# Kernel tuning notes

Measured on AMD Instinct MI355X. Metric: run time of the kernel, lower is better.

The kernel has to match this reference:

```python
import jax, jax.numpy as jnp
import numpy as np

B, C_IN, H, W = 4, 256, 48, 48
HEADS, HD = 8, 64
N = H * W
SCALE = 1.0 / (HD ** 0.5)


def setup_inputs() -> dict:
    key = jax.random.key(0)
    ks = jax.random.split(key, 5)
    x = jax.random.normal(ks[0], (B, C_IN, H, W), dtype=jnp.float32)
    # 1x1 conv weights, squeezed: [heads, head_channels, in_channels]
    Wq = jax.random.normal(ks[1], (HEADS, HD, C_IN), dtype=jnp.float32) * (C_IN ** -0.5)
    Wk = jax.random.normal(ks[2], (HEADS, HD, C_IN), dtype=jnp.float32) * (C_IN ** -0.5)
    Wv = jax.random.normal(ks[3], (HEADS, HD, C_IN), dtype=jnp.float32) * (C_IN ** -0.5)
    # output 1x1 conv: [in_channels, heads*head_channels]
    Wo = jax.random.normal(ks[4], (C_IN, HEADS * HD), dtype=jnp.float32) * ((HEADS * HD) ** -0.5)
    return {"x": x, "Wq": Wq, "Wk": Wk, "Wv": Wv, "Wo": Wo}


def reference(x, Wq, Wk, Wv, Wo):
    b, c, h, w = x.shape
    n = h * w
    xf = x.reshape(b, c, n)  # [B, C, N]
    # per-head 1x1 convs == batched projections -> [heads, B, N, HD]
    q = jnp.einsum('hdc,bcn->hbnd', Wq, xf)
    k = jnp.einsum('hdc,bcn->hbnd', Wk, xf)
    v = jnp.einsum('hdc,bcn->hbnd', Wv, xf)
    scores = jnp.einsum('hbnd,hbmd->hbnm', q, k) * SCALE  # [heads, B, N, N]
    probs = jax.nn.softmax(scores, axis=-1)
    ws = jnp.einsum('hbnm,hbmd->hbnd', probs, v)  # [heads, B, N, HD]
    # faithful replication of torch: transpose(1,2) then reshape(B, heads*HD, H, W)
    ws = jnp.transpose(ws, (0, 2, 1, 3))  # [heads, N, B, HD]
    ws = ws.reshape(b, HEADS * HD, h, w)
    out = jnp.einsum('oc,bchw->bohw', Wo, ws)  # output 1x1 conv
    return out
```

## Files before the change

kernel.cpp:

```cpp
#include <hip/hip_runtime.h>

#define B_     4
#define CIN    256
#define NTOK   2304
#define HEADS  8
#define HD     64
#define SCALE  0.125f
#define LOG2E  1.44269504088896f
#define QSCALE (SCALE * LOG2E)
#define PBIAS  4.0f
#define QKV_ELEMS (HEADS * B_ * NTOK * HD)
#define HBSTRIDE 147456
#define WSZ    131072

typedef _Float16 f16;
typedef _Float16 __attribute__((ext_vector_type(8))) h8v;
typedef _Float16 __attribute__((ext_vector_type(4))) h4v;
typedef ushort   __attribute__((ext_vector_type(8))) us8;
typedef float    __attribute__((ext_vector_type(16))) f16v;

__device__ inline uint pk2(float a, float b) {
    auto v = __builtin_amdgcn_cvt_pkrtz(a, b);
    return __builtin_bit_cast(uint, v);
}
#define EXP2(x) __builtin_amdgcn_exp2f(x)

#define GLOAD_LDS(g, l) __builtin_amdgcn_global_load_lds( \
    (const __attribute__((address_space(1))) unsigned int*)(g), \
    (__attribute__((address_space(3))) unsigned int*)(l), 16, 0, 0)

__global__ __launch_bounds__(256) void castw(
    const float* __restrict__ Wq, const float* __restrict__ Wk,
    const float* __restrict__ Wv, const float* __restrict__ Wo,
    f16* __restrict__ wc, f16* __restrict__ woc)
{
    int e4 = (blockIdx.x * 256 + threadIdx.x) * 4;
    const float* src; f16* dst; float mult = 1.0f; int off;
    if (e4 < WSZ)          { src = Wq; off = e4;           dst = wc;           mult = QSCALE; }
    else if (e4 < 2 * WSZ) { src = Wk; off = e4 - WSZ;     dst = wc + WSZ; }
    else if (e4 < 3 * WSZ) { src = Wv; off = e4 - 2 * WSZ; dst = wc + 2 * WSZ; }
    else                   { src = Wo; off = e4 - 3 * WSZ; dst = woc; }
    float4 r = *(const float4*)(src + off);
    h4v hv;
    hv.x = (f16)(r.x * mult); hv.y = (f16)(r.y * mult);
    hv.z = (f16)(r.z * mult); hv.w = (f16)(r.w * mult);
    *(h4v*)(dst + off) = hv;
}

__global__ __launch_bounds__(256) void tcastf(
    const float* __restrict__ src, f16* __restrict__ dst, int C)
{
    const int n0 = blockIdx.x * 64;
    const int c0 = blockIdx.y * 64;
    const int b  = blockIdx.z;
    __shared__ float T[64][65];
    const int tid = threadIdx.x;
    const float* sb = src + ((size_t)b * C + c0) * NTOK;
    #pragma unroll
    for (int i = 0; i < 16; ++i) {
        int idx = tid + 256 * i;
        int rr = idx >> 6, ll = idx & 63;
        T[ll][rr] = sb[(size_t)rr * NTOK + n0 + ll];
    }
    __syncthreads();
    const size_t ob = ((size_t)b * NTOK + n0) * C + c0;
    #pragma unroll
    for (int i = 0; i < 4; ++i) {
        int idx = tid + 256 * i;
        int row = idx >> 4, c4 = (idx & 15) * 4;
        h4v v;
        v.x = (f16)T[row][c4 + 0]; v.y = (f16)T[row][c4 + 1];
        v.z = (f16)T[row][c4 + 2]; v.w = (f16)T[row][c4 + 3];
        *(h4v*)(dst + ob + (size_t)row * C + c4) = v;
    }
}

__global__ __launch_bounds__(128) void proj_mfma(
    const f16* __restrict__ wc, const f16* __restrict__ xt,
    f16* __restrict__ qh, f16* __restrict__ kh, f16* __restrict__ vth)
{
    const int ntile = blockIdx.x;
    const int hp    = blockIdx.y;
    const int b     = blockIdx.z;
    const int p     = hp >> 3, h = hp & 7;
    const int hb    = h * 4 + b;
    const f16* Wp = wc + ((size_t)p * 8 + h) * (HD * CIN);

    __shared__ __align__(16) f16 Ws[2][64][64], Xs[2][64][64];

    const int tid = threadIdx.x;
    const int w = tid >> 6, lane = tid & 63;
    const int lm = lane & 31, lh = lane >> 5;
    const int n_loc  = w * 32 + lm;
    const int n_glob = ntile * 64 + n_loc;

    const f16* xb = xt + ((size_t)b * NTOK + ntile * 64) * CIN;

    auto stage = [&](int buf, int c0) {
        const f16* src = (w == 0) ? Wp : xb;
        f16* dst = (w == 0) ? &Ws[buf][0][0] : &Xs[buf][0][0];
        #pragma unroll
        for (int i = 0; i < 8; ++i) {
            int g = i * 64 + lane; int row = g >> 3; int c = (g & 7) ^ (row & 7);
            GLOAD_LDS(src + (size_t)row * CIN + c0 + c * 8, dst + i * 512);
        }
    };

    f16v o0, o1;
    #pragma unroll
    for (int i = 0; i < 16; ++i) { o0[i] = 0.f; o1[i] = 0.f; }

    stage(0, 0);
    for (int c0 = 0; c0 < CIN; c0 += 64) {
        const int cur = (c0 >> 6) & 1;
        __syncthreads();
        if (c0 + 64 < CIN) stage(cur ^ 1, c0 + 64);
        #pragma unroll
        for (int s = 0; s < 4; ++s) {
            const int pp = ((2 * s + lh) ^ (lm & 7)) * 8;
            h8v a0 = *(const h8v*)&Ws[cur][lm][pp];
            h8v a1 = *(const h8v*)&Ws[cur][lm + 32][pp];
            h8v bh = *(const h8v*)&Xs[cur][n_loc][pp];
            o0 = __builtin_amdgcn_mfma_f32_32x32x16_f16(a0, bh, o0, 0, 0, 0);
            o1 = __builtin_amdgcn_mfma_f32_32x32x16_f16(a1, bh, o1, 0, 0, 0);
        }
    }

    const size_t hboff = (size_t)hb * HBSTRIDE;
    if (p < 2) {
        f16* oh = ((p == 0) ? qh : kh) + hboff + (size_t)n_glob * 64;
        #pragma unroll
        for (int t = 0; t < 2; ++t) {
            const f16v& oc = t ? o1 : o0;
            #pragma unroll
            for (int g = 0; g < 4; ++g) {
                int d0 = 8 * g + 4 * lh + 32 * t;
                h4v hv;
                hv.x = (f16)oc[4 * g + 0]; hv.y = (f16)oc[4 * g + 1];
                hv.z = (f16)oc[4 * g + 2]; hv.w = (f16)oc[4 * g + 3];
                *(h4v*)(oh + d0) = hv;
            }
        }
    } else {
        f16* oh = vth + hboff;
        #pragma unroll
        for (int t = 0; t < 2; ++t) {
            const f16v& oc = t ? o1 : o0;
            #pragma unroll
            for (int r = 0; r < 16; ++r) {
                int d = (r & 3) + 8 * (r >> 2) + 4 * lh + 32 * t;
                oh[(size_t)d * NTOK + n_glob] = (f16)oc[r];
            }
        }
    }
}

__global__ __launch_bounds__(512, 2) void attn_mfma(
    const f16* __restrict__ qh, const f16* __restrict__ kh,
    const f16* __restrict__ vth, f16* __restrict__ wsth)
{
    const int bid   = blockIdx.x;
    const int xcd   = bid & 7;
    const int slot  = bid >> 3;
    const int hb    = xcd * 4 + (slot / 18);
    const int rpair = slot % 18;
    const int h_    = hb >> 2, b = hb & 3;
    const int tid   = threadIdx.x;
    const int w     = tid >> 6;
    const int lane  = tid & 63;
    const int lm    = lane & 31;
    const int lh    = lane >> 5;
    const int rr    = w >> 1;
    const int ks    = w & 1;

    __shared__ __align__(16) f16 SMEM[2][2][2][64][64];

    const size_t hboff = (size_t)hb * HBSTRIDE;
    const int m = rpair * 128 + rr * 32 + lm;

    h8v Qf[4];
    #pragma unroll
    for (int s = 0; s < 4; ++s)
        Qf[s] = *(const h8v*)(qh + hboff + (size_t)m * 64 + (2 * s + lh) * 8);

    f16v o0, o1;
    #pragma unroll
    for (int i = 0; i < 16; ++i) { o0[i] = 0.f; o1[i] = 0.f; }
    float lsum = 0.f;

    const int  sv    = w >> 2;
    const int  stp   = (w >> 1) & 1;
    const int  shalf = w & 1;
    const f16* gb    = (sv == 0) ? kh + hboff : vth + hboff;

    auto stage = [&](int buf, int st) {
        const int kts = 2 * st + stp;
        f16* dst = &SMEM[buf][sv][stp][0][0];
        #pragma unroll
        for (int j = 0; j < 4; ++j) {
            int i   = shalf * 4 + j;
            int g   = i * 64 + lane;
            int row = g >> 3;
            int c   = (g & 7) ^ (row & 7);
            const f16* src = (sv == 0)
                ? gb + kts * 4096 + row * 64 + c * 8
                : gb + (size_t)row * 2304 + kts * 64 + c * 8;
            GLOAD_LDS(src, dst + i * 512);
        }
    };

    stage(0, 0);
    __syncthreads();

    for (int st = 0; st < 18; ++st) {
        const int cur = st & 1;
        if (st + 1 < 18) stage(cur ^ 1, st + 1);

        f16v s0, s1;
        #pragma unroll
        for (int i = 0; i < 16; ++i) { s0[i] = -PBIAS; s1[i] = -PBIAS; }

        __builtin_amdgcn_s_setprio(1);
        #pragma unroll
        for (int s = 0; s < 4; ++s) {
            const int p = ((2 * s + lh) ^ (lm & 7)) * 8;
            h8v k0 = *(const h8v*)&SMEM[cur][0][ks][lm][p];
            h8v k1 = *(const h8v*)&SMEM[cur][0][ks][lm + 32][p];
            s0 = __builtin_amdgcn_mfma_f32_32x32x16_f16(k0, Qf[s], s0, 0, 0, 0);
            s1 = __builtin_amdgcn_mfma_f32_32x32x16_f16(k1, Qf[s], s1, 0, 0, 0);
        }
        __builtin_amdgcn_s_setprio(0);

        float rs = 0.f;
        #pragma unroll
        for (int i = 0; i < 16; ++i) { s0[i] = EXP2(s0[i]); rs += s0[i]; }
        #pragma unroll
        for (int i = 0; i < 16; ++i) { s1[i] = EXP2(s1[i]); rs += s1[i]; }
        lsum += rs;

        uint Ppk[2][8];
        #pragma unroll
        for (int pr = 0; pr < 8; ++pr) {
            Ppk[0][pr] = pk2(s0[2 * pr], s0[2 * pr + 1]);
            Ppk[1][pr] = pk2(s1[2 * pr], s1[2 * pr + 1]);
        }

        h8v pf[4];
        #pragma unroll
        for (int s = 0; s < 4; ++s) {
            const int jt = s >> 1, q = 4 * (s & 1);
            uint kp0 = lh ? Ppk[jt][q + 2] : Ppk[jt][q + 0];
            uint kp1 = lh ? Ppk[jt][q + 3] : Ppk[jt][q + 1];
            uint sp0 = lh ? Ppk[jt][q + 0] : Ppk[jt][q + 2];
            uint sp1 = lh ? Ppk[jt][q + 1] : Ppk[jt][q + 3];
            uint rp0 = (uint)__shfl_xor((int)sp0, 32);
            uint rp1 = (uint)__shfl_xor((int)sp1, 32);
            uint4 u = { lh ? rp0 : kp0, lh ? rp1 : kp1,
                        lh ? kp0 : rp0, lh ? kp1 : rp1 };
            pf[s] = __builtin_bit_cast(h8v, u);
        }

        __builtin_amdgcn_s_setprio(1);
        #pragma unroll
        for (int s = 0; s < 4; ++s) {
            const int p = ((2 * s + lh) ^ (lm & 7)) * 8;
            h8v v0 = *(const h8v*)&SMEM[cur][1][ks][lm][p];
            h8v v1 = *(const h8v*)&SMEM[cur][1][ks][lm + 32][p];
            o0 = __builtin_amdgcn_mfma_f32_32x32x16_f16(v0, pf[s], o0, 0, 0, 0);
            o1 = __builtin_amdgcn_mfma_f32_32x32x16_f16(v1, pf[s], o1, 0, 0, 0);
        }
        __builtin_amdgcn_s_setprio(0);

        __syncthreads();
    }

    float* red = (float*)&SMEM[0][0][0][0][0];
    if (ks == 1) {
        float* dst = red + (size_t)(rr * 64 + lane) * 33;
        #pragma unroll
        for (int i = 0; i < 16; ++i) { dst[i] = o0[i]; dst[16 + i] = o1[i]; }
        dst[32] = lsum;
    }
    __syncthreads();
    if (ks == 0) {
        const float* sp = red + (size_t)(rr * 64 + lane) * 33;
        #pragma unroll
        for (int i = 0; i < 16; ++i) { o0[i] += sp[i]; o1[i] += sp[16 + i]; }
        lsum += sp[32];
        lsum += __shfl_xor(lsum, 32);
        float inv = 1.0f / lsum;
        f16* wrow = wsth + ((size_t)h_ * NTOK + m) * 256 + b * 64;
        #pragma unroll
        for (int g = 0; g < 4; ++g) {
            h4v r0, r1;
            r0.x = (f16)(o0[4 * g + 0] * inv); r0.y = (f16)(o0[4 * g + 1] * inv);
            r0.z = (f16)(o0[4 * g + 2] * inv); r0.w = (f16)(o0[4 * g + 3] * inv);
            *(h4v*)(wrow + 8 * g + 4 * lh) = r0;
            r1.x = (f16)(o1[4 * g + 0] * inv); r1.y = (f16)(o1[4 * g + 1] * inv);
            r1.z = (f16)(o1[4 * g + 2] * inv); r1.w = (f16)(o1[4 * g + 3] * inv);
            *(h4v*)(wrow + 32 + 8 * g + 4 * lh) = r1;
        }
    }
}

__global__ __launch_bounds__(128) void outconv_mfma(
    const f16* __restrict__ woc, const f16* __restrict__ ws,
    float* __restrict__ out)
{
    const int ntile = blockIdx.x;
    const int otile = blockIdx.y;
    const int b     = blockIdx.z;

    __shared__ __align__(16) f16 Wos[2][64][64];
    __shared__ __align__(16) f16 Xs[2][64][72];

    const int tid = threadIdx.x;
    const int w = tid >> 6, lane = tid & 63;
    const int lm = lane & 31, lh = lane >> 5;
    const int n_loc  = w * 32 + lm;
    const int n_glob = ntile * 64 + n_loc;
    const int pr = tid >> 2;
    const int qn = tid & 3;

    const f16* Wb = woc + (size_t)(otile * 64) * 512;
    const f16* wsb = ws + (size_t)b * 512 * NTOK + ntile * 64 + qn * 16;

    auto stageW = [&](int buf, int c0) {
        #pragma unroll
        for (int j = 0; j < 4; ++j) {
            int i = w * 4 + j;
            int g = i * 64 + lane; int row = g >> 3; int c = (g & 7) ^ (row & 7);
            GLOAD_LDS(Wb + (size_t)row * 512 + c0 + c * 8,
                      &Wos[buf][0][0] + i * 512);
        }
    };

    uint4 x0, x1, x2, x3;
    auto loadB = [&](int c0) {
        const f16* r0 = wsb + (size_t)(c0 + 2 * pr) * NTOK;
        const f16* r1 = r0 + NTOK;
        x0 = *(const uint4*)(r0);
        x1 = *(const uint4*)(r0 + 8);
        x2 = *(const uint4*)(r1);
        x3 = *(const uint4*)(r1 + 8);
    };
    auto storeB = [&](int buf) {
        us8 a0 = __builtin_bit_cast(us8, x0), a1 = __builtin_bit_cast(us8, x1);
        us8 b0 = __builtin_bit_cast(us8, x2), b1 = __builtin_bit_cast(us8, x3);
        #pragma unroll
        for (int j = 0; j < 8; ++j) {
            *(uint*)&Xs[buf][qn * 16 + j][2 * pr]     = (uint)a0[j] | ((uint)b0[j] << 16);
            *(uint*)&Xs[buf][qn * 16 + 8 + j][2 * pr] = (uint)a1[j] | ((uint)b1[j] << 16);
        }
    };

    f16v o0, o1;
    #pragma unroll
    for (int i = 0; i < 16; ++i) { o0[i] = 0.f; o1[i] = 0.f; }

    stageW(0, 0);
    loadB(0);
    storeB(0);
    for (int c0 = 0; c0 < 512; c0 += 64) {
        const int cur = (c0 >> 6) & 1;
        __syncthreads();
        if (c0 + 64 < 512) { stageW(cur ^ 1, c0 + 64); loadB(c0 + 64); }
        #pragma unroll
        for (int s = 0; s < 4; ++s) {
            const int pp = ((2 * s + lh) ^ (lm & 7)) * 8;
            const int co = (2 * s + lh) * 8;
            h8v a0 = *(const h8v*)&Wos[cur][lm][pp];
            h8v a1 = *(const h8v*)&Wos[cur][lm + 32][pp];
            h8v bh = *(const h8v*)&Xs[cur][n_loc][co];
            o0 = __builtin_amdgcn_mfma_f32_32x32x16_f16(a0, bh, o0, 0, 0, 0);
            o1 = __builtin_amdgcn_mfma_f32_32x32x16_f16(a1, bh, o1, 0, 0, 0);
        }
        if (c0 + 64 < 512) storeB(cur ^ 1);
    }

    #pragma unroll
    for (int t = 0; t < 2; ++t) {
        const f16v& oc = t ? o1 : o0;
        #pragma unroll
        for (int r = 0; r < 16; ++r) {
            int orow = otile * 64 + (r & 3) + 8 * (r >> 2) + 4 * lh + 32 * t;
            out[((size_t)b * CIN + orow) * NTOK + n_glob] = oc[r];
        }
    }
}

extern "C" void kernel_launch(void* const* d_in, const int* in_sizes, int n_in,
                              void* d_out, int out_size, void* d_ws, size_t ws_size,
                              hipStream_t stream)
{
    const float* x  = (const float*)d_in[0];
    const float* Wq = (const float*)d_in[1];
    const float* Wk = (const float*)d_in[2];
    const float* Wv = (const float*)d_in[3];
    const float* Wo = (const float*)d_in[4];
    float* out = (float*)d_out;

    f16* qh   = (f16*)d_ws;
    f16* kh   = qh   + QKV_ELEMS;
    f16* vth  = kh   + QKV_ELEMS;
    f16* wsth = vth  + QKV_ELEMS;
    f16* xt   = wsth;
    f16* wc   = wsth + QKV_ELEMS;
    f16* woc  = wc   + 3 * WSZ;

    castw<<<dim3(512), 256, 0, stream>>>(Wq, Wk, Wv, Wo, wc, woc);
    tcastf<<<dim3(36, 4, 4), 256, 0, stream>>>(x, xt, CIN);
    proj_mfma<<<dim3(36, 24, 4), 128, 0, stream>>>(wc, xt, qh, kh, vth);
    attn_mfma<<<dim3(576), 512, 0, stream>>>(qh, kh, vth, wsth);
    outconv_mfma<<<dim3(36, 4, 4), 128, 0, stream>>>(woc, wsth, out);
}
```

Before: 180.2 us.

## Merge prep kernels, single-buffer attention LDS with split K/V staging, use permlane32_swap

The weight cast and input transpose kernels are merged into one prep launch, removing a kernel launch. The attention kernel drops its LDS double buffer. It refills K right after the QK MFMAs and refills V after the PV MFMAs, with an extra barrier per step, which halves LDS use and may raise occupancy. The P fragment shuffle switches from shfl_xor to permlane32_swap, the exp-sum uses four accumulators, and the reduction scratch uses rotated indexing instead of padding. The risk is exposed load latency, since each tile is now loaded only just before it is consumed.

```diff
diff --git a/kernel.cpp b/kernel.cpp
--- a/kernel.cpp
+++ b/kernel.cpp
@@ -29,33 +29,36 @@
     (const __attribute__((address_space(1))) unsigned int*)(g), \
     (__attribute__((address_space(3))) unsigned int*)(l), 16, 0, 0)
 
-__global__ __launch_bounds__(256) void castw(
+__global__ __launch_bounds__(256) void prep(
+    const float* __restrict__ x,
     const float* __restrict__ Wq, const float* __restrict__ Wk,
     const float* __restrict__ Wv, const float* __restrict__ Wo,
-    f16* __restrict__ wc, f16* __restrict__ woc)
+    f16* __restrict__ wc, f16* __restrict__ woc, f16* __restrict__ xt)
 {
-    int e4 = (blockIdx.x * 256 + threadIdx.x) * 4;
-    const float* src; f16* dst; float mult = 1.0f; int off;
-    if (e4 < WSZ)          { src = Wq; off = e4;           dst = wc;           mult = QSCALE; }
-    else if (e4 < 2 * WSZ) { src = Wk; off = e4 - WSZ;     dst = wc + WSZ; }
-    else if (e4 < 3 * WSZ) { src = Wv; off = e4 - 2 * WSZ; dst = wc + 2 * WSZ; }
-    else                   { src = Wo; off = e4 - 3 * WSZ; dst = woc; }
-    float4 r = *(const float4*)(src + off);
-    h4v hv;
-    hv.x = (f16)(r.x * mult); hv.y = (f16)(r.y * mult);
-    hv.z = (f16)(r.z * mult); hv.w = (f16)(r.w * mult);
-    *(h4v*)(dst + off) = hv;
-}
-
-__global__ __launch_bounds__(256) void tcastf(
-    const float* __restrict__ src, f16* __restrict__ dst, int C)
-{
-    const int n0 = blockIdx.x * 64;
-    const int c0 = blockIdx.y * 64;
-    const int b  = blockIdx.z;
     __shared__ float T[64][65];
+    const int bid = blockIdx.x;
     const int tid = threadIdx.x;
-    const float* sb = src + ((size_t)b * C + c0) * NTOK;
+
+    if (bid < 512) {
+        int e4 = (bid * 256 + tid) * 4;
+        const float* src; f16* dst; float mult = 1.0f; int off;
+        if (e4 < WSZ)          { src = Wq; off = e4;           dst = wc;           mult = QSCALE; }
+        else if (e4 < 2 * WSZ) { src = Wk; off = e4 - WSZ;     dst = wc + WSZ; }
+        else if (e4 < 3 * WSZ) { src = Wv; off = e4 - 2 * WSZ; dst = wc + 2 * WSZ; }
+        else                   { src = Wo; off = e4 - 3 * WSZ; dst = woc; }
+        float4 r = *(const float4*)(src + off);
+        h4v hv;
+        hv.x = (f16)(r.x * mult); hv.y = (f16)(r.y * mult);
+        hv.z = (f16)(r.z * mult); hv.w = (f16)(r.w * mult);
+        *(h4v*)(dst + off) = hv;
+        return;
+    }
+
+    const int r  = bid - 512;
+    const int n0 = (r % 36) * 64;
+    const int c0 = ((r / 36) % 4) * 64;
+    const int b  = r / 144;
+    const float* sb = x + ((size_t)b * CIN + c0) * NTOK;
     #pragma unroll
     for (int i = 0; i < 16; ++i) {
         int idx = tid + 256 * i;
@@ -63,7 +66,7 @@
         T[ll][rr] = sb[(size_t)rr * NTOK + n0 + ll];
     }
     __syncthreads();
-    const size_t ob = ((size_t)b * NTOK + n0) * C + c0;
+    const size_t ob = ((size_t)b * NTOK + n0) * CIN + c0;
     #pragma unroll
     for (int i = 0; i < 4; ++i) {
         int idx = tid + 256 * i;
@@ -71,7 +74,7 @@
         h4v v;
         v.x = (f16)T[row][c4 + 0]; v.y = (f16)T[row][c4 + 1];
         v.z = (f16)T[row][c4 + 2]; v.w = (f16)T[row][c4 + 3];
-        *(h4v*)(dst + ob + (size_t)row * C + c4) = v;
+        *(h4v*)(xt + ob + (size_t)row * CIN + c4) = v;
     }
 }
 
@@ -173,7 +176,8 @@
     const int rr    = w >> 1;
     const int ks    = w & 1;
 
-    __shared__ __align__(16) f16 SMEM[2][2][2][64][64];
+    __shared__ __align__(16) f16 SMEM[2][2][64][64];
+    __shared__ float LRED[256];
 
     const size_t hboff = (size_t)hb * HBSTRIDE;
     const int m = rpair * 128 + rr * 32 + lm;
@@ -193,9 +197,9 @@
     const int  shalf = w & 1;
     const f16* gb    = (sv == 0) ? kh + hboff : vth + hboff;
 
-    auto stage = [&](int buf, int st) {
+    auto stage = [&](int st) {
         const int kts = 2 * st + stp;
-        f16* dst = &SMEM[buf][sv][stp][0][0];
+        f16* dst = &SMEM[sv][stp][0][0];
         #pragma unroll
         for (int j = 0; j < 4; ++j) {
             int i   = shalf * 4 + j;
@@ -209,13 +213,10 @@
         }
     };
 
-    stage(0, 0);
+    stage(0);
     __syncthreads();
 
     for (int st = 0; st < 18; ++st) {
-        const int cur = st & 1;
-        if (st + 1 < 18) stage(cur ^ 1, st + 1);
-
         f16v s0, s1;
         #pragma unroll
         for (int i = 0; i < 16; ++i) { s0[i] = -PBIAS; s1[i] = -PBIAS; }
@@ -224,69 +225,83 @@
         #pragma unroll
         for (int s = 0; s < 4; ++s) {
             const int p = ((2 * s + lh) ^ (lm & 7)) * 8;
-            h8v k0 = *(const h8v*)&SMEM[cur][0][ks][lm][p];
-            h8v k1 = *(const h8v*)&SMEM[cur][0][ks][lm + 32][p];
+            h8v k0 = *(const h8v*)&SMEM[0][ks][lm][p];
+            h8v k1 = *(const h8v*)&SMEM[0][ks][lm + 32][p];
             s0 = __builtin_amdgcn_mfma_f32_32x32x16_f16(k0, Qf[s], s0, 0, 0, 0);
             s1 = __builtin_amdgcn_mfma_f32_32x32x16_f16(k1, Qf[s], s1, 0, 0, 0);
         }
         __builtin_amdgcn_s_setprio(0);
 
-        float rs = 0.f;
-        #pragma unroll
-        for (int i = 0; i < 16; ++i) { s0[i] = EXP2(s0[i]); rs += s0[i]; }
-        #pragma unroll
-        for (int i = 0; i < 16; ++i) { s1[i] = EXP2(s1[i]); rs += s1[i]; }
-        lsum += rs;
-
-        uint Ppk[2][8];
-        #pragma unroll
-        for (int pr = 0; pr < 8; ++pr) {
-            Ppk[0][pr] = pk2(s0[2 * pr], s0[2 * pr + 1]);
-            Ppk[1][pr] = pk2(s1[2 * pr], s1[2 * pr + 1]);
-        }
+        __syncthreads();
+        if (st + 1 < 18 && sv == 0) stage(st + 1);
+
+        float p0 = 0.f, p1 = 0.f, p2 = 0.f, p3 = 0.f;
+        #pragma unroll
+        for (int i = 0; i < 16; i += 4) {
+            s0[i+0] = EXP2(s0[i+0]); p0 += s0[i+0];
+            s0[i+1] = EXP2(s0[i+1]); p1 += s0[i+1];
+            s0[i+2] = EXP2(s0[i+2]); p2 += s0[i+2];
+            s0[i+3] = EXP2(s0[i+3]); p3 += s0[i+3];
+        }
+        #pragma unroll
+        for (int i = 0; i < 16; i += 4) {
+            s1[i+0] = EXP2(s1[i+0]); p0 += s1[i+0];
+            s1[i+1] = EXP2(s1[i+1]); p1 += s1[i+1];
+            s1[i+2] = EXP2(s1[i+2]); p2 += s1[i+2];
+            s1[i+3] = EXP2(s1[i+3]); p3 += s1[i+3];
+        }
+        lsum += (p0 + p1) + (p2 + p3);
 
         h8v pf[4];
         #pragma unroll
         for (int s = 0; s < 4; ++s) {
-            const int jt = s >> 1, q = 4 * (s & 1);
-            uint kp0 = lh ? Ppk[jt][q + 2] : Ppk[jt][q + 0];
-            uint kp1 = lh ? Ppk[jt][q + 3] : Ppk[jt][q + 1];
-            uint sp0 = lh ? Ppk[jt][q + 0] : Ppk[jt][q + 2];
-            uint sp1 = lh ? Ppk[jt][q + 1] : Ppk[jt][q + 3];
-            uint rp0 = (uint)__shfl_xor((int)sp0, 32);
-            uint rp1 = (uint)__shfl_xor((int)sp1, 32);
-            uint4 u = { lh ? rp0 : kp0, lh ? rp1 : kp1,
-                        lh ? kp0 : rp0, lh ? kp1 : rp1 };
-            pf[s] = __builtin_bit_cast(h8v, u);
+            const int q2 = 8 * (s & 1);
+            const f16v& ja = (s >> 1) ? s1 : s0;
+            uint a0 = pk2(ja[q2 + 0], ja[q2 + 1]);
+            uint a1 = pk2(ja[q2 + 2], ja[q2 + 3]);
+            uint a2 = pk2(ja[q2 + 4], ja[q2 + 5]);
+            uint a3 = pk2(ja[q2 + 6], ja[q2 + 7]);
+            auto a02 = __builtin_amdgcn_permlane32_swap(a0, a2, false, false);
+            auto a13 = __builtin_amdgcn_permlane32_swap(a1, a3, false, false);
+            uint4 ua = { a02[0], a13[0], a02[1], a13[1] };
+            pf[s] = __builtin_bit_cast(h8v, ua);
         }
 
         __builtin_amdgcn_s_setprio(1);
         #pragma unroll
         for (int s = 0; s < 4; ++s) {
             const int p = ((2 * s + lh) ^ (lm & 7)) * 8;
-            h8v v0 = *(const h8v*)&SMEM[cur][1][ks][lm][p];
-            h8v v1 = *(const h8v*)&SMEM[cur][1][ks][lm + 32][p];
+            h8v v0 = *(const h8v*)&SMEM[1][ks][lm][p];
+            h8v v1 = *(const h8v*)&SMEM[1][ks][lm + 32][p];
             o0 = __builtin_amdgcn_mfma_f32_32x32x16_f16(v0, pf[s], o0, 0, 0, 0);
             o1 = __builtin_amdgcn_mfma_f32_32x32x16_f16(v1, pf[s], o1, 0, 0, 0);
         }
         __builtin_amdgcn_s_setprio(0);
 
         __syncthreads();
-    }
-
-    float* red = (float*)&SMEM[0][0][0][0][0];
+        if (st + 1 < 18 && sv == 1) stage(st + 1);
+    }
+
+    float* red = (float*)&SMEM[0][0][0][0];
+    const int row = rr * 64 + lane;
     if (ks == 1) {
-        float* dst = red + (size_t)(rr * 64 + lane) * 33;
-        #pragma unroll
-        for (int i = 0; i < 16; ++i) { dst[i] = o0[i]; dst[16 + i] = o1[i]; }
-        dst[32] = lsum;
+        float* d = red + (size_t)row * 32;
+        #pragma unroll
+        for (int i = 0; i < 16; ++i) {
+            d[(i + row) & 31] = o0[i];
+            d[(16 + i + row) & 31] = o1[i];
+        }
+        LRED[row] = lsum;
     }
     __syncthreads();
     if (ks == 0) {
-        const float* sp = red + (size_t)(rr * 64 + lane) * 33;
-        #pragma unroll
-        for (int i = 0; i < 16; ++i) { o0[i] += sp[i]; o1[i] += sp[16 + i]; }
-        lsum += sp[32];
+        const float* sp = red + (size_t)row * 32;
+        #pragma unroll
+        for (int i = 0; i < 16; ++i) {
+            o0[i] += sp[(i + row) & 31];
+            o1[i] += sp[(16 + i + row) & 31];
+        }
+        lsum += LRED[row];
         lsum += __shfl_xor(lsum, 32);
         float inv = 1.0f / lsum;
         f16* wrow = wsth + ((size_t)h_ * NTOK + m) * 256 + b * 64;
@@ -408,8 +423,7 @@
     f16* wc   = wsth + QKV_ELEMS;
     f16* woc  = wc   + 3 * WSZ;
 
-    castw<<<dim3(512), 256, 0, stream>>>(Wq, Wk, Wv, Wo, wc, woc);
-    tcastf<<<dim3(36, 4, 4), 256, 0, stream>>>(x, xt, CIN);
+    prep<<<dim3(1088), 256, 0, stream>>>(x, Wq, Wk, Wv, Wo, wc, woc, xt);
     proj_mfma<<<dim3(36, 24, 4), 128, 0, stream>>>(wc, xt, qh, kh, vth);
     attn_mfma<<<dim3(576), 512, 0, stream>>>(qh, kh, vth, wsth);
     outconv_mfma<<<dim3(36, 4, 4), 128, 0, stream>>>(woc, wsth, out);
```

Result: no change. 177.5 us (-1.5%).
